# Optimization experiments

Hardware: AMD Instinct MI355X
Metric: run time of the kernel (lower is better)

The kernel has to match this reference:

```python
import jax, jax.numpy as jnp
import numpy as np

N_TOKENS = 8192
NQ = 6
NL = 2


def ry_mat(theta):
    # theta: scalar or (B,) -> (2,2) or (B,2,2) complex RY matrix
    c = jnp.cos(theta / 2)
    s = jnp.sin(theta / 2)
    return jnp.stack([jnp.stack([c, -s], -1), jnp.stack([s, c], -1)], -2).astype(jnp.complex64)


def apply_1q(state, gate, q, nq):
    # state: (B, 2**nq); gate: (2,2) shared or (B,2,2) per-batch
    B = state.shape[0]
    st = state.reshape(B, 2 ** q, 2, -1)
    if gate.ndim == 3:
        st = jnp.einsum('bij,bajc->baic', gate, st)
    else:
        st = jnp.einsum('ij,bajc->baic', gate, st)
    return st.reshape(B, -1)


def apply_rz(state, theta, q, nq):
    # diagonal RZ: multiply phases, no matmul needed
    B = state.shape[0]
    st = state.reshape(B, 2 ** q, 2, -1)
    ph = jnp.stack([jnp.exp(-0.5j * theta), jnp.exp(0.5j * theta)]).astype(jnp.complex64)
    return (st * ph[None, None, :, None]).reshape(B, -1)


def apply_cnot(state, c, t, nq):
    B = state.shape[0]
    st = state.reshape((B,) + (2,) * nq)
    s0 = jnp.take(st, 0, axis=1 + c)
    s1 = jnp.take(st, 1, axis=1 + c)
    ta = 1 + t - (1 if t > c else 0)  # target axis after removing control axis
    s1 = jnp.flip(s1, axis=ta)
    st = jnp.stack([s0, s1], axis=1 + c)
    return st.reshape(B, -1)


def prepare_states(x, params, nl, nq):
    # x: (B, nq) angles; params: (nl, nq, 2). Returns (B, 2**nq) complex statevectors.
    B = x.shape[0]
    state = jnp.zeros((B, 2 ** nq), jnp.complex64).at[:, 0].set(1.0)
    for q in range(nq):  # RY angle embedding
        state = apply_1q(state, ry_mat(x[:, q]), q, nq)
    for l in range(nl):  # PQC layers: RY, RZ rotations + CNOT ring
        for q in range(nq):
            state = apply_1q(state, ry_mat(params[l, q, 0]), q, nq)
            state = apply_rz(state, params[l, q, 1], q, nq)
        for q in range(nq):
            state = apply_cnot(state, q, (q + 1) % nq, nq)
    return state


def setup_inputs() -> dict:
    key = jax.random.key(0)
    k1, k2, k3, k4 = jax.random.split(key, 4)
    return {
        'x_tokens': jax.random.normal(k1, (N_TOKENS, NQ), dtype=jnp.float32),
        'params_q': 0.1 * jax.random.normal(k2, (NL, NQ, 2), dtype=jnp.float32),
        'params_k': 0.1 * jax.random.normal(k3, (NL, NQ, 2), dtype=jnp.float32),
        'params_v': 0.1 * jax.random.normal(k4, (NL, NQ, 2), dtype=jnp.float32),
    }


def reference(x_tokens, params_q, params_k, params_v):
    nq = x_tokens.shape[1]
    nl = params_q.shape[0]
    sq = prepare_states(x_tokens, params_q, nl, nq)  # (N, 2**nq)
    sk = prepare_states(x_tokens, params_k, nl, nq)
    ov = jnp.einsum('id,jd->ij', sq, jnp.conj(sk))  # pairwise overlaps (N, N)
    logits = jnp.real(ov * jnp.conj(ov))            # swap-test fidelity |<q|k>|^2
    attn = jax.nn.softmax(logits, axis=-1)
    sv = prepare_states(x_tokens, params_v, nl, nq)
    probs = jnp.real(sv * jnp.conj(sv))             # (N, 2**nq)
    idx = jnp.arange(2 ** nq)
    bits = (idx[None, :] >> (nq - 1 - jnp.arange(nq))[:, None]) & 1  # (nq, 2**nq)
    signs = (1.0 - 2.0 * bits).astype(probs.dtype)
    V = probs @ signs.T                              # <Z_q> per qubit -> (N, nq)
    return attn @ V
```

## Files before the change

kernel.cpp:

```cpp
#include <hip/hip_runtime.h>
#include <hip/hip_bf16.h>
#include <hip/hip_fp16.h>

#define NT 8192
#define NQB 6
#define NL 2
#define JSPLIT 16
#define JSLICE (NT / JSPLIT)
#define CHUNK 32
#define NCHUNK (JSLICE / CHUNK)
#define IPW 16
#define WPB 4
#define IPB (IPW * WPB)
#define NBI (NT / IPB)
#define WSTRIDE 40

typedef _Float16 f16x8 __attribute__((ext_vector_type(8)));
typedef float f32x4 __attribute__((ext_vector_type(4)));

static __device__ __forceinline__ unsigned int pack_h2(float a, float b) {
  unsigned short lo = __builtin_bit_cast(unsigned short, (_Float16)a);
  unsigned short hi = __builtin_bit_cast(unsigned short, (_Float16)b);
  return (unsigned int)lo | ((unsigned int)hi << 16);
}

static __device__ __forceinline__ int cnot_src(int p, int q) {
  const int mc = 1 << (5 - q);
  const int mt = 1 << (5 - ((q + 1) % NQB));
  return (p & mc) ? (p ^ mt) : p;
}

#define GLOAD_LDS16(g, l)                                      \
  __builtin_amdgcn_global_load_lds(                            \
      (const __attribute__((address_space(1))) void*)(g),      \
      (__attribute__((address_space(3))) void*)(l), 16, 0, 0)

__global__ __launch_bounds__(256) void prep_kernel(
    const float* __restrict__ x, const float* __restrict__ pq,
    const float* __restrict__ pk, const float* __restrict__ pv,
    unsigned int* __restrict__ Are, unsigned int* __restrict__ Bk,
    unsigned short* __restrict__ Vt)
{
  const int wid  = blockIdx.x * 4 + (threadIdx.x >> 6);
  const int lane = threadIdx.x & 63;
  const int set  = wid >> 13;
  const int tok  = wid & (NT - 1);
  const float* pp = (set == 0) ? pq : ((set == 1) ? pk : pv);

  int m = lane;
#pragma unroll
  for (int q = 5; q >= 0; --q) m = cnot_src(m, q);
  int inv = lane;
#pragma unroll
  for (int q = 0; q < 6; ++q) inv = cnot_src(inv, q);

  float R = 1.f, phi = 0.f;
#pragma unroll
  for (int q = 0; q < 6; ++q) {
    float s, c;
    __sincosf(0.5f * (x[tok * NQB + q] + pp[q * 2 + 0]), &s, &c);
    const float bh = 0.5f * pp[q * 2 + 1];
    if ((m >> (5 - q)) & 1) { R *= s; phi += bh; }
    else                    { R *= c; phi -= bh; }
  }
  float sp, cp;
  __sincosf(phi, &sp, &cp);
  float re = R * cp, im = R * sp;

#pragma unroll
  for (int q = 0; q < 6; ++q) {
    const int mask = 1 << (5 - q);
    float s, c;
    __sincosf(0.5f * pp[2 * NQB + q * 2 + 0], &s, &c);
    const float pre = __shfl_xor(re, mask, 64);
    const float pim = __shfl_xor(im, mask, 64);
    const float se = (lane & mask) ? s : -s;
    re = fmaf(se, pre, c * re);
    im = fmaf(se, pim, c * im);
  }
  float phi2 = 0.f;
#pragma unroll
  for (int q = 0; q < 6; ++q) {
    const float bh = 0.5f * pp[2 * NQB + q * 2 + 1];
    phi2 += (lane & (1 << (5 - q))) ? bh : -bh;
  }
  float s2, c2;
  __sincosf(phi2, &s2, &c2);
  const float fre = re * c2 - im * s2;
  const float fim = re * s2 + im * c2;

  if (set == 0) {
    Are[tok * 64 + inv] = pack_h2(fre, fim);
  } else if (set == 1) {
    const int sidx = ((((inv >> 2) ^ (tok & 15)) << 2) | (inv & 3));
    Bk[tok * 64 + sidx] = pack_h2(fre, fim);
  } else {
    const float prob = fre * fre + fim * fim;
    float vq[NQB];
#pragma unroll
    for (int q = 0; q < NQB; ++q) {
      float v = (inv & (1 << (5 - q))) ? -prob : prob;
#pragma unroll
      for (int off = 1; off < 64; off <<= 1) v += __shfl_xor(v, off, 64);
      vq[q] = v;
    }
    if (lane < 16) {
      const int q = lane & 7;
      float sel = vq[0];
      if (q == 1) sel = vq[1];
      if (q == 2) sel = vq[2];
      if (q == 3) sel = vq[3];
      if (q == 4) sel = vq[4];
      if (q == 5) sel = vq[5];
      if (q == 6) sel = 1.0f;
      if (q == 7) sel = 0.0f;
      float outv;
      if (lane < 8) {
        outv = sel;
      } else {
        const float hi = (float)(_Float16)sel;
        outv = (q < 6) ? (sel - hi) : 0.0f;
      }
      Vt[lane * NT + tok] = __builtin_bit_cast(unsigned short, (_Float16)outv);
    }
  }
}

__global__ __launch_bounds__(256, 2) void attn_kernel(
    const uint4* __restrict__ Are, const uint4* __restrict__ Bk,
    const unsigned short* __restrict__ Vt, float* __restrict__ part)
{
  __shared__ uint4 kbuf[2][CHUNK * 16];
  __shared__ __align__(16) unsigned short wbuf[WPB][16][WSTRIDE];

  const int tid  = threadIdx.x;
  const int lane = tid & 63;
  const int wave = tid >> 6;
  const int col  = lane & 15;
  const int quad = lane >> 4;

  const int ib = blockIdx.x & (NBI - 1);
  const int js = blockIdx.x >> 7;
  const int ibase = ib * IPB + wave * IPW;
  const int jbase0 = js * JSLICE;

  f16x8 qRe[4], qIm[4];
  {
    const uint4* pr = Are + (ibase + col) * 16 + quad;
#pragma unroll
    for (int s = 0; s < 4; ++s) {
      const uint4 u = pr[s * 4];
      uint4 w;
      w.x = ((u.x << 16) | (u.x >> 16)) ^ 0x80000000u;
      w.y = ((u.y << 16) | (u.y >> 16)) ^ 0x80000000u;
      w.z = ((u.z << 16) | (u.z >> 16)) ^ 0x80000000u;
      w.w = ((u.w << 16) | (u.w >> 16)) ^ 0x80000000u;
      qRe[s] = __builtin_bit_cast(f16x8, u);
      qIm[s] = __builtin_bit_cast(f16x8, w);
    }
  }

  int koff[4];
#pragma unroll
  for (int s = 0; s < 4; ++s) koff[s] = (((s * 4 + quad) ^ col) << 4);

  f32x4 acc = {0.f, 0.f, 0.f, 0.f};

  auto stage = [&](int buf, int c) {
#pragma unroll
    for (int r = 0; r < 2; ++r) {
      const int slot = wave * 2 + r;
      GLOAD_LDS16(Bk + (size_t)(jbase0 + c * CHUNK) * 16 + slot * 64 + lane,
                  &kbuf[buf][slot * 64]);
    }
  };

  stage(0, 0);

#pragma unroll 1
  for (int c = 0; c < NCHUNK; ++c) {
    const int cur = c & 1;
    const int jb = jbase0 + c * CHUNK;
    const f16x8 vb = *(const f16x8*)(Vt + (size_t)col * NT + jb + quad * 8);
    if (c + 1 < NCHUNK) {
      stage(cur ^ 1, c + 1);
      asm volatile("s_waitcnt vmcnt(2)" ::: "memory");
    } else {
      asm volatile("s_waitcnt vmcnt(0)" ::: "memory");
    }
    __builtin_amdgcn_s_barrier();

#pragma unroll
    for (int ct = 0; ct < 2; ++ct) {
      const char* kb = (const char*)kbuf[cur] + (ct * 16 + col) * 256;
      f16x8 bfr[4];
#pragma unroll
      for (int s = 0; s < 4; ++s) bfr[s] = *(const f16x8*)(kb + koff[s]);
      f32x4 aR = {0.f, 0.f, 0.f, 0.f};
      f32x4 aI = {0.f, 0.f, 0.f, 0.f};
#pragma unroll
      for (int s = 0; s < 4; ++s) {
        aR = __builtin_amdgcn_mfma_f32_16x16x32_f16(bfr[s], qRe[s], aR, 0, 0, 0);
        aI = __builtin_amdgcn_mfma_f32_16x16x32_f16(bfr[s], qIm[s], aI, 0, 0, 0);
      }
      const float w0 = __expf(aR[0] * aR[0] + aI[0] * aI[0]);
      const float w1 = __expf(aR[1] * aR[1] + aI[1] * aI[1]);
      const float w2 = __expf(aR[2] * aR[2] + aI[2] * aI[2]);
      const float w3 = __expf(aR[3] * aR[3] + aI[3] * aI[3]);
      *(uint2*)&wbuf[wave][col][ct * 16 + quad * 4] =
          make_uint2(pack_h2(w0, w1), pack_h2(w2, w3));
    }
    const f16x8 wA = *(const f16x8*)&wbuf[wave][col][quad * 8];
    acc = __builtin_amdgcn_mfma_f32_16x16x32_f16(wA, vb, acc, 0, 0, 0);
    __builtin_amdgcn_s_barrier();
  }

  float res[4];
#pragma unroll
  for (int r = 0; r < 4; ++r) res[r] = acc[r] + __shfl_xor(acc[r], 8, 64);
  if (col < 8) {
    float* p = part + ((size_t)(js * NT + ibase + quad * 4)) * 8 + col;
#pragma unroll
    for (int r = 0; r < 4; ++r) p[r * 8] = res[r];
  }
}

__global__ __launch_bounds__(256) void combine_kernel(
    const float* __restrict__ part, float* __restrict__ out)
{
  const int row = blockIdx.x * 256 + threadIdx.x;
  float acc[7] = {0.f, 0.f, 0.f, 0.f, 0.f, 0.f, 0.f};
#pragma unroll
  for (int js = 0; js < JSPLIT; ++js) {
    const float* p = part + ((size_t)(js * NT + row)) * 8;
#pragma unroll
    for (int q = 0; q < 7; ++q) acc[q] += p[q];
  }
  const float inv = 1.0f / acc[6];
#pragma unroll
  for (int q = 0; q < 6; ++q)
    out[row * 6 + q] = acc[q] * inv;
}

extern "C" void kernel_launch(void* const* d_in, const int* in_sizes, int n_in,
                              void* d_out, int out_size, void* d_ws, size_t ws_size,
                              hipStream_t stream) {
  const float* x  = (const float*)d_in[0];
  const float* pq = (const float*)d_in[1];
  const float* pk = (const float*)d_in[2];
  const float* pv = (const float*)d_in[3];
  char* ws = (char*)d_ws;
  unsigned int*   Are = (unsigned int*)(ws);
  unsigned int*   Bk  = (unsigned int*)(ws + (size_t)(2u << 20));
  unsigned short* Vt  = (unsigned short*)(ws + (size_t)(4u << 20));
  float*          prt = (float*)(ws + (size_t)(4u << 20) + (size_t)(256u << 10));

  prep_kernel<<<(NT * 3) / 4, 256, 0, stream>>>(x, pq, pk, pv, Are, Bk, Vt);
  attn_kernel<<<NBI * JSPLIT, 256, 0, stream>>>((const uint4*)Are, (const uint4*)Bk,
                                                Vt, prt);
  combine_kernel<<<NT / 256, 256, 0, stream>>>(prt, (float*)d_out);
}
```

Measured before the change: 131.7 us.

## Precompute trig tables in separate kernel and restructure attention chunk pipeline

```diff
diff --git a/kernel.cpp b/kernel.cpp
--- a/kernel.cpp
+++ b/kernel.cpp
@@ -24,6 +24,10 @@
   return (unsigned int)lo | ((unsigned int)hi << 16);
 }
 
+static __device__ __forceinline__ unsigned int pkrtz(float a, float b) {
+  return __builtin_bit_cast(unsigned int, __builtin_amdgcn_cvt_pkrtz(a, b));
+}
+
 static __device__ __forceinline__ int cnot_src(int p, int q) {
   const int mc = 1 << (5 - q);
   const int mt = 1 << (5 - ((q + 1) % NQB));
@@ -35,9 +39,60 @@
       (const __attribute__((address_space(1))) void*)(g),      \
       (__attribute__((address_space(3))) void*)(l), 16, 0, 0)
 
-__global__ __launch_bounds__(256) void prep_kernel(
+__global__ __launch_bounds__(256) void precomp_kernel(
     const float* __restrict__ x, const float* __restrict__ pq,
     const float* __restrict__ pk, const float* __restrict__ pv,
+    float2* __restrict__ xsc, float2* __restrict__ phtab,
+    float2* __restrict__ rytab)
+{
+  const int gid = blockIdx.x * 256 + threadIdx.x;
+  if (gid < NT * NQB) {
+    float s, c;
+    __sincosf(0.5f * x[gid], &s, &c);
+    xsc[gid] = make_float2(s, c);
+    return;
+  }
+  const int t = gid - NT * NQB;
+  if (t < 3 * 128) {
+    const int set  = t >> 7;
+    const int r    = t & 127;
+    const int lane = r & 63;
+    const int which = r >> 6;
+    const float* pp = (set == 0) ? pq : ((set == 1) ? pk : pv);
+    float phi = 0.f;
+    if (which == 0) {
+      int m = lane;
+#pragma unroll
+      for (int q = 5; q >= 0; --q) m = cnot_src(m, q);
+#pragma unroll
+      for (int q = 0; q < 6; ++q) {
+        const float bh = 0.5f * pp[q * 2 + 1];
+        phi += ((m >> (5 - q)) & 1) ? bh : -bh;
+      }
+    } else {
+#pragma unroll
+      for (int q = 0; q < 6; ++q) {
+        const float bh = 0.5f * pp[12 + q * 2 + 1];
+        phi += ((lane >> (5 - q)) & 1) ? bh : -bh;
+      }
+    }
+    float s, c;
+    __sincosf(phi, &s, &c);
+    phtab[t] = make_float2(c, s);
+  } else if (t < 3 * 128 + 36) {
+    const int i = t - 3 * 128;
+    const int set = i / 12, r = i % 12;
+    const float* pp = (set == 0) ? pq : ((set == 1) ? pk : pv);
+    const int layer = r / 6, q = r % 6;
+    float s, c;
+    __sincosf(0.5f * pp[layer * 12 + q * 2], &s, &c);
+    rytab[i] = make_float2(s, c);
+  }
+}
+
+__global__ __launch_bounds__(256) void prep_kernel(
+    const float2* __restrict__ xsc, const float2* __restrict__ phtab,
+    const float2* __restrict__ rytab,
     unsigned int* __restrict__ Are, unsigned int* __restrict__ Bk,
     unsigned short* __restrict__ Vt)
 {
@@ -45,7 +100,6 @@
   const int lane = threadIdx.x & 63;
   const int set  = wid >> 13;
   const int tok  = wid & (NT - 1);
-  const float* pp = (set == 0) ? pq : ((set == 1) ? pk : pv);
 
   int m = lane;
 #pragma unroll
@@ -54,40 +108,34 @@
 #pragma unroll
   for (int q = 0; q < 6; ++q) inv = cnot_src(inv, q);
 
-  float R = 1.f, phi = 0.f;
+  const float2* xs = xsc + tok * NQB;
+  const float2* ry = rytab + set * 12;
+
+  float R = 1.f;
 #pragma unroll
   for (int q = 0; q < 6; ++q) {
-    float s, c;
-    __sincosf(0.5f * (x[tok * NQB + q] + pp[q * 2 + 0]), &s, &c);
-    const float bh = 0.5f * pp[q * 2 + 1];
-    if ((m >> (5 - q)) & 1) { R *= s; phi += bh; }
-    else                    { R *= c; phi -= bh; }
-  }
-  float sp, cp;
-  __sincosf(phi, &sp, &cp);
-  float re = R * cp, im = R * sp;
+    const float2 tq = xs[q];
+    const float2 pr = ry[q];
+    const float s = tq.x * pr.y + tq.y * pr.x;
+    const float c = tq.y * pr.y - tq.x * pr.x;
+    R *= ((m >> (5 - q)) & 1) ? s : c;
+  }
+  const float2 ph0 = phtab[set * 128 + lane];
+  float re = R * ph0.x, im = R * ph0.y;
 
 #pragma unroll
   for (int q = 0; q < 6; ++q) {
     const int mask = 1 << (5 - q);
-    float s, c;
-    __sincosf(0.5f * pp[2 * NQB + q * 2 + 0], &s, &c);
+    const float2 rc = ry[6 + q];
     const float pre = __shfl_xor(re, mask, 64);
     const float pim = __shfl_xor(im, mask, 64);
-    const float se = (lane & mask) ? s : -s;
-    re = fmaf(se, pre, c * re);
-    im = fmaf(se, pim, c * im);
-  }
-  float phi2 = 0.f;
-#pragma unroll
-  for (int q = 0; q < 6; ++q) {
-    const float bh = 0.5f * pp[2 * NQB + q * 2 + 1];
-    phi2 += (lane & (1 << (5 - q))) ? bh : -bh;
-  }
-  float s2, c2;
-  __sincosf(phi2, &s2, &c2);
-  const float fre = re * c2 - im * s2;
-  const float fim = re * s2 + im * c2;
+    const float se = (lane & mask) ? rc.x : -rc.x;
+    re = fmaf(se, pre, rc.y * re);
+    im = fmaf(se, pim, rc.y * im);
+  }
+  const float2 ph1 = phtab[set * 128 + 64 + lane];
+  const float fre = re * ph1.x - im * ph1.y;
+  const float fim = re * ph1.y + im * ph1.x;
 
   if (set == 0) {
     Are[tok * 64 + inv] = pack_h2(fre, fim);
@@ -176,19 +224,16 @@
   };
 
   stage(0, 0);
+  asm volatile("s_waitcnt vmcnt(0)" ::: "memory");
+  __builtin_amdgcn_s_barrier();
+  asm volatile("" ::: "memory");
 
 #pragma unroll 1
   for (int c = 0; c < NCHUNK; ++c) {
     const int cur = c & 1;
     const int jb = jbase0 + c * CHUNK;
+    if (c + 1 < NCHUNK) stage(cur ^ 1, c + 1);
     const f16x8 vb = *(const f16x8*)(Vt + (size_t)col * NT + jb + quad * 8);
-    if (c + 1 < NCHUNK) {
-      stage(cur ^ 1, c + 1);
-      asm volatile("s_waitcnt vmcnt(2)" ::: "memory");
-    } else {
-      asm volatile("s_waitcnt vmcnt(0)" ::: "memory");
-    }
-    __builtin_amdgcn_s_barrier();
 
 #pragma unroll
     for (int ct = 0; ct < 2; ++ct) {
@@ -208,11 +253,16 @@
       const float w2 = __expf(aR[2] * aR[2] + aI[2] * aI[2]);
       const float w3 = __expf(aR[3] * aR[3] + aI[3] * aI[3]);
       *(uint2*)&wbuf[wave][col][ct * 16 + quad * 4] =
-          make_uint2(pack_h2(w0, w1), pack_h2(w2, w3));
+          make_uint2(pkrtz(w0, w1), pkrtz(w2, w3));
     }
     const f16x8 wA = *(const f16x8*)&wbuf[wave][col][quad * 8];
     acc = __builtin_amdgcn_mfma_f32_16x16x32_f16(wA, vb, acc, 0, 0, 0);
-    __builtin_amdgcn_s_barrier();
+
+    if (c + 1 < NCHUNK) {
+      asm volatile("s_waitcnt vmcnt(0)" ::: "memory");
+      __builtin_amdgcn_s_barrier();
+      asm volatile("" ::: "memory");
+    }
   }
 
   float res[4];
@@ -253,9 +303,15 @@
   unsigned int*   Are = (unsigned int*)(ws);
   unsigned int*   Bk  = (unsigned int*)(ws + (size_t)(2u << 20));
   unsigned short* Vt  = (unsigned short*)(ws + (size_t)(4u << 20));
-  float*          prt = (float*)(ws + (size_t)(4u << 20) + (size_t)(256u << 10));
-
-  prep_kernel<<<(NT * 3) / 4, 256, 0, stream>>>(x, pq, pk, pv, Are, Bk, Vt);
+  char*           partb = ws + (size_t)(4u << 20) + (size_t)(256u << 10);
+  float*          prt = (float*)partb;
+  float2*         xsc   = (float2*)partb;
+  float2*         phtab = (float2*)(partb + (size_t)(384u << 10));
+  float2*         rytab = (float2*)(partb + (size_t)(384u << 10) + 4096);
+
+  const int pre_grid = (NT * NQB + 3 * 128 + 36 + 255) / 256;
+  precomp_kernel<<<pre_grid, 256, 0, stream>>>(x, pq, pk, pv, xsc, phtab, rytab);
+  prep_kernel<<<(NT * 3) / 4, 256, 0, stream>>>(xsc, phtab, rytab, Are, Bk, Vt);
   attn_kernel<<<NBI * JSPLIT, 256, 0, stream>>>((const uint4*)Are, (const uint4*)Bk,
                                                 Vt, prt);
   combine_kernel<<<NT / 256, 256, 0, stream>>>(prt, (float*)d_out);
```

Result: no change. 134.3 us (+2.0%).

## Double query rows per wave, reuse K fragments, and pipeline the weight MFMA

Applied to the files above, without the earlier changes.

```diff
diff --git a/kernel.cpp b/kernel.cpp
--- a/kernel.cpp
+++ b/kernel.cpp
@@ -9,7 +9,7 @@
 #define JSLICE (NT / JSPLIT)
 #define CHUNK 32
 #define NCHUNK (JSLICE / CHUNK)
-#define IPW 16
+#define IPW 32
 #define WPB 4
 #define IPB (IPW * WPB)
 #define NBI (NT / IPB)
@@ -22,6 +22,10 @@
   unsigned short lo = __builtin_bit_cast(unsigned short, (_Float16)a);
   unsigned short hi = __builtin_bit_cast(unsigned short, (_Float16)b);
   return (unsigned int)lo | ((unsigned int)hi << 16);
+}
+
+static __device__ __forceinline__ unsigned int pkrtz(float a, float b) {
+  return __builtin_bit_cast(unsigned int, __builtin_amdgcn_cvt_pkrtz(a, b));
 }
 
 static __device__ __forceinline__ int cnot_src(int p, int q) {
@@ -54,40 +58,52 @@
 #pragma unroll
   for (int q = 0; q < 6; ++q) inv = cnot_src(inv, q);
 
-  float R = 1.f, phi = 0.f;
+  float a = 0.f;
+  if (lane < 6)                    a = 0.5f * x[tok * NQB + lane];
+  else if (lane >= 8 && lane < 14) a = 0.5f * pp[(lane - 8) * 2];
+  else if (lane >= 16 && lane < 22) a = 0.5f * pp[12 + (lane - 16) * 2];
+  float sa, ca;
+  __sincosf(a, &sa, &ca);
+
+  float R = 1.f;
 #pragma unroll
   for (int q = 0; q < 6; ++q) {
-    float s, c;
-    __sincosf(0.5f * (x[tok * NQB + q] + pp[q * 2 + 0]), &s, &c);
+    const float tqs = __shfl(sa, q, 64),     tqc = __shfl(ca, q, 64);
+    const float prs = __shfl(sa, 8 + q, 64), prc = __shfl(ca, 8 + q, 64);
+    const float s = tqs * prc + tqc * prs;
+    const float c = tqc * prc - tqs * prs;
+    R *= ((m >> (5 - q)) & 1) ? s : c;
+  }
+  float phi0 = 0.f;
+#pragma unroll
+  for (int q = 0; q < 6; ++q) {
     const float bh = 0.5f * pp[q * 2 + 1];
-    if ((m >> (5 - q)) & 1) { R *= s; phi += bh; }
-    else                    { R *= c; phi -= bh; }
-  }
-  float sp, cp;
-  __sincosf(phi, &sp, &cp);
-  float re = R * cp, im = R * sp;
+    phi0 += ((m >> (5 - q)) & 1) ? bh : -bh;
+  }
+  float s0, c0;
+  __sincosf(phi0, &s0, &c0);
+  float re = R * c0, im = R * s0;
 
 #pragma unroll
   for (int q = 0; q < 6; ++q) {
     const int mask = 1 << (5 - q);
-    float s, c;
-    __sincosf(0.5f * pp[2 * NQB + q * 2 + 0], &s, &c);
+    const float rcs = __shfl(sa, 16 + q, 64), rcc = __shfl(ca, 16 + q, 64);
     const float pre = __shfl_xor(re, mask, 64);
     const float pim = __shfl_xor(im, mask, 64);
-    const float se = (lane & mask) ? s : -s;
-    re = fmaf(se, pre, c * re);
-    im = fmaf(se, pim, c * im);
-  }
-  float phi2 = 0.f;
+    const float se = (lane & mask) ? rcs : -rcs;
+    re = fmaf(se, pre, rcc * re);
+    im = fmaf(se, pim, rcc * im);
+  }
+  float phi1 = 0.f;
 #pragma unroll
   for (int q = 0; q < 6; ++q) {
-    const float bh = 0.5f * pp[2 * NQB + q * 2 + 1];
-    phi2 += (lane & (1 << (5 - q))) ? bh : -bh;
-  }
-  float s2, c2;
-  __sincosf(phi2, &s2, &c2);
-  const float fre = re * c2 - im * s2;
-  const float fim = re * s2 + im * c2;
+    const float bh = 0.5f * pp[12 + q * 2 + 1];
+    phi1 += ((lane >> (5 - q)) & 1) ? bh : -bh;
+  }
+  float s1, c1;
+  __sincosf(phi1, &s1, &c1);
+  const float fre = re * c1 - im * s1;
+  const float fim = re * s1 + im * c1;
 
   if (set == 0) {
     Are[tok * 64 + inv] = pack_h2(fre, fim);
@@ -131,7 +147,7 @@
     const unsigned short* __restrict__ Vt, float* __restrict__ part)
 {
   __shared__ uint4 kbuf[2][CHUNK * 16];
-  __shared__ __align__(16) unsigned short wbuf[WPB][16][WSTRIDE];
+  __shared__ __align__(16) unsigned short wbuf[2][WPB][2][16][WSTRIDE];
 
   const int tid  = threadIdx.x;
   const int lane = tid & 63;
@@ -140,31 +156,23 @@
   const int quad = lane >> 4;
 
   const int ib = blockIdx.x & (NBI - 1);
-  const int js = blockIdx.x >> 7;
+  const int js = blockIdx.x >> 6;
   const int ibase = ib * IPB + wave * IPW;
   const int jbase0 = js * JSLICE;
 
-  f16x8 qRe[4], qIm[4];
-  {
-    const uint4* pr = Are + (ibase + col) * 16 + quad;
-#pragma unroll
-    for (int s = 0; s < 4; ++s) {
-      const uint4 u = pr[s * 4];
-      uint4 w;
-      w.x = ((u.x << 16) | (u.x >> 16)) ^ 0x80000000u;
-      w.y = ((u.y << 16) | (u.y >> 16)) ^ 0x80000000u;
-      w.z = ((u.z << 16) | (u.z >> 16)) ^ 0x80000000u;
-      w.w = ((u.w << 16) | (u.w >> 16)) ^ 0x80000000u;
-      qRe[s] = __builtin_bit_cast(f16x8, u);
-      qIm[s] = __builtin_bit_cast(f16x8, w);
-    }
+  f16x8 qRe[2][4];
+#pragma unroll
+  for (int rt = 0; rt < 2; ++rt) {
+    const uint4* pr = Are + (ibase + rt * 16 + col) * 16 + quad;
+#pragma unroll
+    for (int s = 0; s < 4; ++s) qRe[rt][s] = __builtin_bit_cast(f16x8, pr[s * 4]);
   }
 
   int koff[4];
 #pragma unroll
   for (int s = 0; s < 4; ++s) koff[s] = (((s * 4 + quad) ^ col) << 4);
 
-  f32x4 acc = {0.f, 0.f, 0.f, 0.f};
+  f32x4 acc[2] = {{0.f, 0.f, 0.f, 0.f}, {0.f, 0.f, 0.f, 0.f}};
 
   auto stage = [&](int buf, int c) {
 #pragma unroll
@@ -176,52 +184,85 @@
   };
 
   stage(0, 0);
-
+  asm volatile("s_waitcnt vmcnt(0)" ::: "memory");
+  __builtin_amdgcn_s_barrier();
+  asm volatile("" ::: "memory");
+
+  f16x8 vb_prev;
 #pragma unroll 1
   for (int c = 0; c < NCHUNK; ++c) {
     const int cur = c & 1;
     const int jb = jbase0 + c * CHUNK;
+    if (c + 1 < NCHUNK) stage(cur ^ 1, c + 1);
     const f16x8 vb = *(const f16x8*)(Vt + (size_t)col * NT + jb + quad * 8);
-    if (c + 1 < NCHUNK) {
-      stage(cur ^ 1, c + 1);
-      asm volatile("s_waitcnt vmcnt(2)" ::: "memory");
-    } else {
-      asm volatile("s_waitcnt vmcnt(0)" ::: "memory");
-    }
-    __builtin_amdgcn_s_barrier();
+    f16x8 wA0, wA1;
+    if (c > 0) {
+      wA0 = *(const f16x8*)&wbuf[cur ^ 1][wave][0][col][quad * 8];
+      wA1 = *(const f16x8*)&wbuf[cur ^ 1][wave][1][col][quad * 8];
+    }
 
 #pragma unroll
     for (int ct = 0; ct < 2; ++ct) {
       const char* kb = (const char*)kbuf[cur] + (ct * 16 + col) * 256;
-      f16x8 bfr[4];
-#pragma unroll
-      for (int s = 0; s < 4; ++s) bfr[s] = *(const f16x8*)(kb + koff[s]);
-      f32x4 aR = {0.f, 0.f, 0.f, 0.f};
-      f32x4 aI = {0.f, 0.f, 0.f, 0.f};
+      f16x8 bfr[4], bfi[4];
 #pragma unroll
       for (int s = 0; s < 4; ++s) {
-        aR = __builtin_amdgcn_mfma_f32_16x16x32_f16(bfr[s], qRe[s], aR, 0, 0, 0);
-        aI = __builtin_amdgcn_mfma_f32_16x16x32_f16(bfr[s], qIm[s], aI, 0, 0, 0);
+        const uint4 u = *(const uint4*)(kb + koff[s]);
+        uint4 w;
+        w.x = ((u.x << 16) | (u.x >> 16)) ^ 0x00008000u;
+        w.y = ((u.y << 16) | (u.y >> 16)) ^ 0x00008000u;
+        w.z = ((u.z << 16) | (u.z >> 16)) ^ 0x00008000u;
+        w.w = ((u.w << 16) | (u.w >> 16)) ^ 0x00008000u;
+        bfr[s] = __builtin_bit_cast(f16x8, u);
+        bfi[s] = __builtin_bit_cast(f16x8, w);
       }
-      const float w0 = __expf(aR[0] * aR[0] + aI[0] * aI[0]);
-      const float w1 = __expf(aR[1] * aR[1] + aI[1] * aI[1]);
-      const float w2 = __expf(aR[2] * aR[2] + aI[2] * aI[2]);
-      const float w3 = __expf(aR[3] * aR[3] + aI[3] * aI[3]);
-      *(uint2*)&wbuf[wave][col][ct * 16 + quad * 4] =
-          make_uint2(pack_h2(w0, w1), pack_h2(w2, w3));
-    }
-    const f16x8 wA = *(const f16x8*)&wbuf[wave][col][quad * 8];
-    acc = __builtin_amdgcn_mfma_f32_16x16x32_f16(wA, vb, acc, 0, 0, 0);
-    __builtin_amdgcn_s_barrier();
-  }
-
-  float res[4];
-#pragma unroll
-  for (int r = 0; r < 4; ++r) res[r] = acc[r] + __shfl_xor(acc[r], 8, 64);
-  if (col < 8) {
-    float* p = part + ((size_t)(js * NT + ibase + quad * 4)) * 8 + col;
-#pragma unroll
-    for (int r = 0; r < 4; ++r) p[r * 8] = res[r];
+#pragma unroll
+      for (int rt = 0; rt < 2; ++rt) {
+        f32x4 aR = {0.f, 0.f, 0.f, 0.f};
+        f32x4 aI = {0.f, 0.f, 0.f, 0.f};
+#pragma unroll
+        for (int s = 0; s < 4; ++s) {
+          aR = __builtin_amdgcn_mfma_f32_16x16x32_f16(bfr[s], qRe[rt][s], aR, 0, 0, 0);
+          aI = __builtin_amdgcn_mfma_f32_16x16x32_f16(bfi[s], qRe[rt][s], aI, 0, 0, 0);
+        }
+        const float w0 = __expf(aR[0] * aR[0] + aI[0] * aI[0]);
+        const float w1 = __expf(aR[1] * aR[1] + aI[1] * aI[1]);
+        const float w2 = __expf(aR[2] * aR[2] + aI[2] * aI[2]);
+        const float w3 = __expf(aR[3] * aR[3] + aI[3] * aI[3]);
+        *(uint2*)&wbuf[cur][wave][rt][col][ct * 16 + quad * 4] =
+            make_uint2(pkrtz(w0, w1), pkrtz(w2, w3));
+      }
+    }
+    if (c > 0) {
+      acc[0] = __builtin_amdgcn_mfma_f32_16x16x32_f16(wA0, vb_prev, acc[0], 0, 0, 0);
+      acc[1] = __builtin_amdgcn_mfma_f32_16x16x32_f16(wA1, vb_prev, acc[1], 0, 0, 0);
+    }
+    vb_prev = vb;
+
+    if (c + 1 < NCHUNK) {
+      asm volatile("s_waitcnt vmcnt(0)" ::: "memory");
+      __builtin_amdgcn_s_barrier();
+      asm volatile("" ::: "memory");
+    }
+  }
+  {
+    const int cur = (NCHUNK - 1) & 1;
+    const f16x8 wA0 = *(const f16x8*)&wbuf[cur][wave][0][col][quad * 8];
+    const f16x8 wA1 = *(const f16x8*)&wbuf[cur][wave][1][col][quad * 8];
+    acc[0] = __builtin_amdgcn_mfma_f32_16x16x32_f16(wA0, vb_prev, acc[0], 0, 0, 0);
+    acc[1] = __builtin_amdgcn_mfma_f32_16x16x32_f16(wA1, vb_prev, acc[1], 0, 0, 0);
+  }
+
+#pragma unroll
+  for (int rt = 0; rt < 2; ++rt) {
+    float res[4];
+#pragma unroll
+    for (int r = 0; r < 4; ++r) res[r] = acc[rt][r] + __shfl_xor(acc[rt][r], 8, 64);
+    if (col < 8) {
+      float* p = part + ((size_t)(js * NT + ibase + rt * 16 + quad * 4)) * 8 + col;
+#pragma unroll
+      for (int r = 0; r < 4; ++r) p[r * 8] = res[r];
+    }
   }
 }
 
```

Result: slower. 135.0 us (+2.5%).
